# Kernel optimization log

Hardware: AMD Instinct MI355X
Metric: run time of the kernel (lower is better)

Reference implementation:

```python
import jax, jax.numpy as jnp
import numpy as np
import math

GROUPS = 32
EPS = 1e-5

def group_norm(x, w, b):
    B, C, H, W = x.shape
    xg = x.reshape(B, GROUPS, C // GROUPS, H, W)
    mu = xg.mean(axis=(2, 3, 4), keepdims=True)
    var = xg.var(axis=(2, 3, 4), keepdims=True)
    xn = ((xg - mu) * jax.lax.rsqrt(var + EPS)).reshape(B, C, H, W)
    return xn * w[None, :, None, None] + b[None, :, None, None]

def conv1x1(x, w, b):
    # x: [B,Cin,H,W], w: [Cout,Cin], b: [Cout]
    return jnp.einsum('bchw,oc->bohw', x, w) + b[None, :, None, None]

def setup_inputs() -> dict:
    key = jax.random.key(0)
    ks = jax.random.split(key, 8)
    B, C, E, H, W = 8, 256, 512, 64, 64
    x = jax.random.normal(ks[0], (B, C, H, W), dtype=jnp.float32)
    condA = jax.random.normal(ks[1], (B, E, H, W), dtype=jnp.float32)
    gn_x_w = jnp.ones((C,), jnp.float32)
    gn_x_b = jnp.zeros((C,), jnp.float32)
    gn_c_w = jnp.ones((E,), jnp.float32)
    gn_c_b = jnp.zeros((E,), jnp.float32)
    q_w = jax.random.normal(ks[2], (C, C), jnp.float32) * 0.02
    q_b = jnp.zeros((C,), jnp.float32)
    k_w = jax.random.normal(ks[3], (C, E), jnp.float32) * 0.02
    k_b = jnp.zeros((C,), jnp.float32)
    v_w = jax.random.normal(ks[4], (C, E), jnp.float32) * 0.02
    v_b = jnp.zeros((C,), jnp.float32)
    return {"x": x, "condA": condA, "gn_x_w": gn_x_w, "gn_x_b": gn_x_b,
            "gn_c_w": gn_c_w, "gn_c_b": gn_c_b, "q_w": q_w, "q_b": q_b,
            "k_w": k_w, "k_b": k_b, "v_w": v_w, "v_b": v_b}

def reference(x, condA, gn_x_w, gn_x_b, gn_c_w, gn_c_b, q_w, q_b, k_w, k_b, v_w, v_b):
    B, C, H, W = x.shape
    scale = math.sqrt(C)
    h = group_norm(x, gn_x_w, gn_x_b)
    h1 = group_norm(condA, gn_c_w, gn_c_b)
    q = conv1x1(h, q_w, q_b)      # [B,C,H,W]
    k = conv1x1(h1, k_w, k_b)     # [B,C,Hc,Wc]
    v = conv1x1(h1, v_w, v_b)     # [B,C,Hc,Wc]
    qf = q.transpose(0, 2, 3, 1).reshape(B, H * W, C)        # [B,N,C]
    kf = k.reshape(B, C, -1)                                  # [B,C,M]
    vf = v.transpose(0, 2, 3, 1).reshape(B, -1, C)            # [B,M,C]
    attn = jax.nn.softmax(jnp.einsum('bnc,bcm->bnm', qf, kf) / scale, axis=-1)
    out = jnp.einsum('bnm,bmc->bnc', attn, vf)                # [B,N,C]
    return out.reshape(B, H, W, C).transpose(0, 3, 1, 2)
```

## Files before the change

kernel.cpp:

```cpp
#include <hip/hip_runtime.h>


typedef _Float16 half8 __attribute__((ext_vector_type(8)));
typedef _Float16 half4v __attribute__((ext_vector_type(4)));
typedef _Float16 half2v __attribute__((ext_vector_type(2)));
typedef float f32x4 __attribute__((ext_vector_type(4)));
typedef float f32x16 __attribute__((ext_vector_type(16)));
typedef unsigned u32x4v __attribute__((ext_vector_type(4)));

#define MFMA16(a, b, c) __builtin_amdgcn_mfma_f32_16x16x32_f16((a), (b), (c), 0, 0, 0)
#define MFMA32(a, b, c) __builtin_amdgcn_mfma_f32_32x32x16_f16((a), (b), (c), 0, 0, 0)

__global__ __launch_bounds__(256) void statswconv_kernel(
    const float* __restrict__ x, const float* __restrict__ condA,
    float* __restrict__ sx, float* __restrict__ sc,
    const float* __restrict__ wq, const float* __restrict__ wk,
    const float* __restrict__ wv, _Float16* __restrict__ wqt,
    _Float16* __restrict__ wkt, _Float16* __restrict__ wvt) {
  int bid = blockIdx.x;
  int t = threadIdx.x;
  if (bid >= 512) {
    int i = (bid - 512) * 256 + t;
    const float* src;
    _Float16* dst;
    int cin, ksbits, gi;
    if (i < 8192) { src = wq; dst = wqt; cin = 256; ksbits = 3; gi = i; }
    else if (i < 24576) { src = wk; dst = wkt; cin = 512; ksbits = 4; gi = i - 8192; }
    else { src = wv; dst = wvt; cin = 512; ksbits = 4; gi = i - 24576; }
    int tile = gi >> 6, g = gi & 63;
    int otile = tile >> ksbits, ks = tile & ((1 << ksbits) - 1);
    int o = otile * 16 + (g & 15), k = ks * 32 + (g >> 4) * 8;
    const float* s = src + (size_t)o * cin + k;
    half8 hv;
#pragma unroll
    for (int j = 0; j < 8; j++) hv[j] = (_Float16)s[j];
    *(half8*)(dst + (size_t)gi * 8) = hv;
    return;
  }
  const float4* src;
  int nf4;
  float* dst;
  float inv_n;
  if (bid < 256) {
    src = (const float4*)(x + (size_t)bid * 32768);
    nf4 = 8192;
    dst = sx + bid * 2;
    inv_n = 1.0f / 32768.0f;
  } else {
    int j = bid - 256;
    src = (const float4*)(condA + (size_t)j * 65536);
    nf4 = 16384;
    dst = sc + j * 2;
    inv_n = 1.0f / 65536.0f;
  }
  float s = 0.f, s2 = 0.f;
  for (int i = t; i < nf4; i += 256) {
    float4 v = src[i];
    s += v.x + v.y + v.z + v.w;
    s2 += v.x * v.x + v.y * v.y + v.z * v.z + v.w * v.w;
  }
#pragma unroll
  for (int m = 1; m <= 32; m <<= 1) {
    s += __shfl_xor(s, m, 64);
    s2 += __shfl_xor(s2, m, 64);
  }
  __shared__ float red[8];
  int w = t >> 6;
  if ((t & 63) == 0) { red[w * 2] = s; red[w * 2 + 1] = s2; }
  __syncthreads();
  if (t == 0) {
    float S = red[0] + red[2] + red[4] + red[6];
    float S2 = red[1] + red[3] + red[5] + red[7];
    float mu = S * inv_n;
    float var = S2 * inv_n - mu * mu;
    dst[0] = mu;
    dst[1] = rsqrtf(var + 1e-5f);
  }
}

__global__ __launch_bounds__(256) void ntrans_kernel(
    const float* __restrict__ x, const float* __restrict__ condA,
    const float* __restrict__ statsx, const float* __restrict__ statsc,
    const float* __restrict__ gxw, const float* __restrict__ gxb,
    const float* __restrict__ gcw, const float* __restrict__ gcb,
    _Float16* __restrict__ hxTt, _Float16* __restrict__ h1Tt) {
  int bid = blockIdx.x;
  const float *src, *stats, *gw, *gb;
  _Float16* dst;
  int CH, gsh, bid2;
  if (bid < 2048) {
    src = x; stats = statsx; gw = gxw; gb = gxb; dst = hxTt;
    CH = 256; gsh = 3; bid2 = bid;
  } else {
    src = condA; stats = statsc; gw = gcw; gb = gcb; dst = h1Tt;
    CH = 512; gsh = 4; bid2 = bid - 2048;
  }
  int b = bid2 & 7, nt = (bid2 >> 3) & 63, ctile = bid2 >> 9;
  int n0 = nt * 64, c0 = ctile * 64;
  int t = threadIdx.x;
  __shared__ float tile[64][65];

  int cl = t >> 2;
  int c = c0 + cl;
  const float* st = stats + ((size_t)b * 32 + (c >> gsh)) * 2;
  float mu = st[0], rs = st[1];
  float a = rs * gw[c];
  float bb = gb[c] - mu * a;
  const float* srow = src + ((size_t)(b * CH + c)) * 4096 + n0 + (t & 3) * 16;
#pragma unroll
  for (int i = 0; i < 4; i++) {
    float4 v = *(const float4*)(srow + 4 * i);
    int nn = (t & 3) * 16 + 4 * i;
    tile[cl][nn + 0] = v.x * a + bb;
    tile[cl][nn + 1] = v.y * a + bb;
    tile[cl][nn + 2] = v.z * a + bb;
    tile[cl][nn + 3] = v.w * a + bb;
  }
  __syncthreads();
  int nl = t >> 2;
  half8 ov[2];
#pragma unroll
  for (int u = 0; u < 2; u++)
#pragma unroll
    for (int i = 0; i < 8; i++) ov[u][i] = (_Float16)tile[(t & 3) * 16 + 8 * u + i][nl];
  int n = n0 + nl;
  size_t tb = ((size_t)b * 256 + (n >> 4)) * (CH >> 5);
  int ca = c0 + (t & 3) * 16;
#pragma unroll
  for (int u = 0; u < 2; u++) {
    int cc = ca + 8 * u;
    size_t addr = ((tb + (cc >> 5)) * 64 + (n & 15) + 16 * ((cc >> 3) & 3)) * 8;
    *(half8*)(dst + addr) = ov[u];
  }
}

__global__ __launch_bounds__(256, 2) void projQ_kernel(
    const _Float16* __restrict__ Ht, const _Float16* __restrict__ Wt,
    const float* __restrict__ bias, _Float16* __restrict__ Qt) {
  int bid = blockIdx.x;
  int b = bid & 7, nt = bid >> 3;
  int t = threadIdx.x, l = t & 63, w = t >> 6;
  int c15 = l & 15, q = l >> 4;

  __shared__ __align__(16) _Float16 hbuf[16384];
  half8* hb = (half8*)hbuf;
  {
    const half8* sg = (const half8*)Ht + (size_t)(b * 256 + nt * 4) * 512;
#pragma unroll
    for (int i = 0; i < 8; i++) hb[t + 256 * i] = sg[t + 256 * i];
  }
  __syncthreads();

  const half8* wt8 = (const half8*)Wt;
#pragma unroll
  for (int p = 0; p < 2; p++) {
    int oa = (p * 4 + w) * 2;
    f32x4 acc[2][4] = {};
#pragma unroll
    for (int ks = 0; ks < 8; ks++) {
      half8 af0 = wt8[((size_t)(oa + 0) * 8 + ks) * 64 + l];
      half8 af1 = wt8[((size_t)(oa + 1) * 8 + ks) * 64 + l];
#pragma unroll
      for (int nt2 = 0; nt2 < 4; nt2++) {
        half8 bf = hb[(nt2 * 8 + ks) * 64 + l];
        acc[0][nt2] = MFMA16(af0, bf, acc[0][nt2]);
        acc[1][nt2] = MFMA16(af1, bf, acc[1][nt2]);
      }
    }
#pragma unroll
    for (int j = 0; j < 2; j++) {
      int o4 = (oa + j) * 16 + 4 * q;
      f32x4 bv = *(const f32x4*)(bias + o4);
#pragma unroll
      for (int nt2 = 0; nt2 < 4; nt2++) {
        half4v hv;
#pragma unroll
        for (int r = 0; r < 4; r++) hv[r] = (_Float16)((acc[j][nt2][r] + bv[r]) * 0.0625f);
        size_t addr = ((((size_t)b * 128 + nt * 2 + (nt2 >> 1)) * 16 + (oa + j)) * 64 +
                       (nt2 & 1) * 16 + c15 + 32 * (q >> 1)) * 8 + (q & 1) * 4;
        *(half4v*)(Qt + addr) = hv;
      }
    }
  }
}

__global__ __launch_bounds__(256, 2) void projKV_kernel(
    const _Float16* __restrict__ Ht, const _Float16* __restrict__ Wk,
    const _Float16* __restrict__ Wv, const float* __restrict__ kb,
    const float* __restrict__ vb, _Float16* __restrict__ Kt,
    _Float16* __restrict__ Vt) {
  int bid = blockIdx.x;
  int b = bid & 7, mt = bid >> 3;
  int m0 = mt * 64;
  int t = threadIdx.x, l = t & 63, w = t >> 6;
  int c15 = l & 15, q = l >> 4;

  __shared__ __align__(16) _Float16 hbuf[32768];
  half8* hb = (half8*)hbuf;
  {
    const half8* sg = (const half8*)Ht + (size_t)(b * 256 + mt * 4) * 1024;
#pragma unroll
    for (int i = 0; i < 16; i++) hb[t + 256 * i] = sg[t + 256 * i];
  }
  __syncthreads();

  const half8* wk8 = (const half8*)Wk;
  const half8* wv8 = (const half8*)Wv;
#pragma unroll
  for (int p = 0; p < 2; p++) {
    int oa = (p * 4 + w) * 2;
    f32x4 acck[2][4] = {};
    f32x4 accv[4][2] = {};
#pragma unroll
    for (int ks = 0; ks < 16; ks++) {
      half8 kf0 = wk8[((size_t)(oa + 0) * 16 + ks) * 64 + l];
      half8 kf1 = wk8[((size_t)(oa + 1) * 16 + ks) * 64 + l];
      half8 vf0 = wv8[((size_t)(oa + 0) * 16 + ks) * 64 + l];
      half8 vf1 = wv8[((size_t)(oa + 1) * 16 + ks) * 64 + l];
#pragma unroll
      for (int nt2 = 0; nt2 < 4; nt2++) {
        half8 lf = hb[(nt2 * 16 + ks) * 64 + l];
        acck[0][nt2] = MFMA16(kf0, lf, acck[0][nt2]);
        acck[1][nt2] = MFMA16(kf1, lf, acck[1][nt2]);
        accv[nt2][0] = MFMA16(lf, vf0, accv[nt2][0]);
        accv[nt2][1] = MFMA16(lf, vf1, accv[nt2][1]);
      }
    }
#pragma unroll
    for (int j = 0; j < 2; j++) {
      int o4 = (oa + j) * 16 + 4 * q;
      f32x4 bv = *(const f32x4*)(kb + o4);
#pragma unroll
      for (int nt2 = 0; nt2 < 4; nt2++) {
        half4v hv;
#pragma unroll
        for (int r = 0; r < 4; r++) hv[r] = (_Float16)(acck[j][nt2][r] + bv[r]);
        size_t addr = ((((size_t)b * 128 + mt * 2 + (nt2 >> 1)) * 16 + (oa + j)) * 64 +
                       (nt2 & 1) * 16 + c15 + 32 * (q >> 1)) * 8 + (q & 1) * 4;
        *(half4v*)(Kt + addr) = hv;
      }
    }
#pragma unroll
    for (int nt2 = 0; nt2 < 4; nt2++) {
      int m = m0 + nt2 * 16 + 4 * q;
      size_t mbase = ((size_t)b * 256 + (m >> 4)) * 8;
#pragma unroll
      for (int j = 0; j < 2; j++) {
        int c = (oa + j) * 16 + c15;
        float bs = vb[c];
        half4v hv;
#pragma unroll
        for (int r = 0; r < 4; r++) hv[r] = (_Float16)(accv[nt2][j][r] + bs);
        size_t addr = ((mbase + (c >> 5)) * 64 + (c & 31) + ((q >> 1) << 5)) * 8 + (q & 1) * 4;
        *(half4v*)(Vt + addr) = hv;
      }
    }
  }
}

__global__ __launch_bounds__(256, 2) void attn_kernel(
    const _Float16* __restrict__ Qt, const _Float16* __restrict__ Kt,
    const _Float16* __restrict__ Vt, float* __restrict__ out,
    float* __restrict__ O1, float* __restrict__ l0g,
    float* __restrict__ l1g) {
  int bid = blockIdx.x;
  int b = bid & 7, nt = bid >> 3;
  int n0 = nt * 64;
  int t = threadIdx.x, l = t & 63, w = t >> 6;
  int l31 = l & 31, h = l >> 5;
  int mh = w & 1, nh = w >> 1;

  __shared__ __align__(16) _Float16 qlds[16384];
  half8* ql8 = (half8*)qlds;
  {
    const half8* sg = (const half8*)Qt + (size_t)(b * 128 + nt * 2) * 1024;
#pragma unroll
    for (int i = 0; i < 8; i++) ql8[t + 256 * i] = sg[t + 256 * i];
  }
  __syncthreads();

  const half8* kt8 = (const half8*)Kt + (size_t)b * 131072 + mh * 1024 + l;
  const half8* vt8 = (const half8*)Vt + (size_t)b * 131072 + l;
  const half8* qw8 = ql8 + nh * 1024 + l;

  f32x16 acc[8] = {};
  float l_part = 0.f;

  for (int it = 0; it < 64; it++) {
    const half8* kb = kt8 + (size_t)it * 2048;

    f32x16 s = {};
#pragma unroll
    for (int g = 0; g < 4; g++) {
      half8 kf[4], qb[4];
#pragma unroll
      for (int i = 0; i < 4; i++) kf[i] = kb[(g * 4 + i) * 64];
#pragma unroll
      for (int i = 0; i < 4; i++) qb[i] = qw8[(g * 4 + i) * 64];
      __builtin_amdgcn_s_setprio(1);
#pragma unroll
      for (int i = 0; i < 4; i++) s = MFMA32(kf[i], qb[i], s);
      __builtin_amdgcn_s_setprio(0);
    }

    unsigned uo[8];
#pragma unroll
    for (int k2 = 0; k2 < 8; k2++) {
      float e0 = __expf(s[2 * k2]);
      float e1 = __expf(s[2 * k2 + 1]);
      l_part += e0 + e1;
      half2v h2 = {(_Float16)e0, (_Float16)e1};
      uo[k2] = __builtin_bit_cast(unsigned, h2);
    }
    unsigned x0 = uo[0], y0 = uo[2];
    asm("v_permlane32_swap_b32 %0, %1" : "+v"(x0), "+v"(y0));
    unsigned x1 = uo[1], y1 = uo[3];
    asm("v_permlane32_swap_b32 %0, %1" : "+v"(x1), "+v"(y1));
    unsigned x2 = uo[4], y2 = uo[6];
    asm("v_permlane32_swap_b32 %0, %1" : "+v"(x2), "+v"(y2));
    unsigned x3 = uo[5], y3 = uo[7];
    asm("v_permlane32_swap_b32 %0, %1" : "+v"(x3), "+v"(y3));
    u32x4v P0 = {x0, x1, y0, y1};
    u32x4v P1 = {x2, x3, y2, y3};
    half8 pf0 = __builtin_bit_cast(half8, P0);
    half8 pf1 = __builtin_bit_cast(half8, P1);

    const half8* vb0 = vt8 + (size_t)((it * 4 + mh * 2) * 8) * 64;
#pragma unroll
    for (int u = 0; u < 2; u++) {
      const half8* vb = vb0 + u * 512;
      half8 pfu = u ? pf1 : pf0;
#pragma unroll
      for (int g = 0; g < 2; g++) {
        half8 vf[4];
#pragma unroll
        for (int i = 0; i < 4; i++) vf[i] = vb[(g * 4 + i) * 64];
        __builtin_amdgcn_s_setprio(1);
#pragma unroll
        for (int i = 0; i < 4; i++)
          acc[g * 4 + i] = MFMA32(pfu, vf[i], acc[g * 4 + i]);
        __builtin_amdgcn_s_setprio(0);
      }
    }
  }

  {
    float v = l_part + __shfl_xor(l_part, 32, 64);
    float* lG = mh ? l1g : l0g;
    if (l < 32) lG[b * 4096 + n0 + nh * 32 + l] = v;
  }
  float* ob = mh ? O1 : out;
#pragma unroll
  for (int cb = 0; cb < 8; cb++) {
    int c = cb * 32 + l31;
    float* orow = ob + ((size_t)(b * 256 + c)) * 4096 + n0 + nh * 32 + 4 * h;
#pragma unroll
    for (int k2 = 0; k2 < 4; k2++) {
      f32x4 o4;
#pragma unroll
      for (int r = 0; r < 4; r++) o4[r] = acc[cb][4 * k2 + r];
      *(f32x4*)(orow + 8 * k2) = o4;
    }
  }
}

__global__ __launch_bounds__(256) void combine_kernel(
    float* __restrict__ out, const float* __restrict__ O1,
    const float* __restrict__ l0g, const float* __restrict__ l1g) {
  size_t i = (size_t)blockIdx.x * 256 + threadIdx.x;
  f32x4 a = ((const f32x4*)out)[i];
  f32x4 b4 = ((const f32x4*)O1)[i];
  int bidx = (int)(i >> 18);
  int n4 = (int)(i & 1023);
  f32x4 La = ((const f32x4*)l0g)[bidx * 1024 + n4];
  f32x4 Lb = ((const f32x4*)l1g)[bidx * 1024 + n4];
  f32x4 r;
#pragma unroll
  for (int j = 0; j < 4; j++) r[j] = (a[j] + b4[j]) / (La[j] + Lb[j]);
  ((f32x4*)out)[i] = r;
}

extern "C" void kernel_launch(void* const* d_in, const int* in_sizes, int n_in,
                              void* d_out, int out_size, void* d_ws,
                              size_t ws_size, hipStream_t stream) {
  const float* x = (const float*)d_in[0];
  const float* condA = (const float*)d_in[1];
  const float* gxw = (const float*)d_in[2];
  const float* gxb = (const float*)d_in[3];
  const float* gcw = (const float*)d_in[4];
  const float* gcb = (const float*)d_in[5];
  const float* qw = (const float*)d_in[6];
  const float* qb = (const float*)d_in[7];
  const float* kw = (const float*)d_in[8];
  const float* kb = (const float*)d_in[9];
  const float* vw = (const float*)d_in[10];
  const float* vb = (const float*)d_in[11];
  float* out = (float*)d_out;

  char* ws = (char*)d_ws;
  float* statsx = (float*)(ws);
  float* statsc = (float*)(ws + 2048);
  _Float16* wqt = (_Float16*)(ws + 4096);
  _Float16* wkt = (_Float16*)(ws + 135168);
  _Float16* wvt = (_Float16*)(ws + 397312);
  char* p = ws + 659456;
  _Float16* hxTt = (_Float16*)p; p += (size_t)8 * 4096 * 256 * 2;
  _Float16* h1Tt = (_Float16*)p; p += (size_t)8 * 4096 * 512 * 2;
  _Float16* Qt = (_Float16*)p;   p += (size_t)8 * 4096 * 256 * 2;
  _Float16* Kt = (_Float16*)p;   p += (size_t)8 * 4096 * 256 * 2;
  _Float16* Vt = (_Float16*)p;

  float* O1 = (float*)(ws + 659456);
  float* l0g = (float*)(ws + 659456 + (size_t)33554432);
  float* l1g = (float*)(ws + 659456 + (size_t)33554432 + 131072);

  statswconv_kernel<<<672, 256, 0, stream>>>(x, condA, statsx, statsc,
                                             qw, kw, vw, wqt, wkt, wvt);
  ntrans_kernel<<<6144, 256, 0, stream>>>(x, condA, statsx, statsc,
                                          gxw, gxb, gcw, gcb, hxTt, h1Tt);
  projQ_kernel<<<512, 256, 0, stream>>>(hxTt, wqt, qb, Qt);
  projKV_kernel<<<512, 256, 0, stream>>>(h1Tt, wkt, wvt, kb, vb, Kt, Vt);
  attn_kernel<<<512, 256, 0, stream>>>(Qt, Kt, Vt, out, O1, l0g, l1g);
  combine_kernel<<<8192, 256, 0, stream>>>(out, O1, l0g, l1g);
}
```

Baseline: 411.0 us.

## Double-buffer K/V tiles in LDS via async global-to-LDS loads in attention

The attention kernel now uses 512-thread blocks that each cover 128 query rows. Q fragments are held in registers instead of LDS. Each K and V tile is staged once per block into double-buffered LDS with global_load_lds, so the next tile's copy overlaps compute on the current one. This shares K/V global traffic across more query rows and hides load latency, at the cost of 128KB of LDS, higher register pressure from the Q fragments, a barrier per iteration, and half as many blocks.

```diff
diff --git a/kernel.cpp b/kernel.cpp
--- a/kernel.cpp
+++ b/kernel.cpp
@@ -10,6 +10,11 @@
 
 #define MFMA16(a, b, c) __builtin_amdgcn_mfma_f32_16x16x32_f16((a), (b), (c), 0, 0, 0)
 #define MFMA32(a, b, c) __builtin_amdgcn_mfma_f32_32x32x16_f16((a), (b), (c), 0, 0, 0)
+
+#define GLOAD_LDS(src, dst)                                                   \
+  __builtin_amdgcn_global_load_lds(                                           \
+      (const __attribute__((address_space(1))) unsigned*)(src),               \
+      (__attribute__((address_space(3))) unsigned*)(dst), 16, 0, 0)
 
 __global__ __launch_bounds__(256) void statswconv_kernel(
     const float* __restrict__ x, const float* __restrict__ condA,
@@ -258,48 +263,67 @@
   }
 }
 
-__global__ __launch_bounds__(256, 2) void attn_kernel(
+__global__ __launch_bounds__(512, 2) void attn_kernel(
     const _Float16* __restrict__ Qt, const _Float16* __restrict__ Kt,
     const _Float16* __restrict__ Vt, float* __restrict__ out,
     float* __restrict__ O1, float* __restrict__ l0g,
     float* __restrict__ l1g) {
   int bid = blockIdx.x;
-  int b = bid & 7, nt = bid >> 3;
-  int n0 = nt * 64;
+  int b = bid & 7, nt2 = bid >> 3;
+  int n0 = nt2 * 128;
   int t = threadIdx.x, l = t & 63, w = t >> 6;
   int l31 = l & 31, h = l >> 5;
   int mh = w & 1, nh = w >> 1;
 
-  __shared__ __align__(16) _Float16 qlds[16384];
-  half8* ql8 = (half8*)qlds;
+  __shared__ __align__(16) _Float16 kbuf[2][16384];
+  __shared__ __align__(16) _Float16 vbuf[2][16384];
+
+  half8 qf[16];
   {
-    const half8* sg = (const half8*)Qt + (size_t)(b * 128 + nt * 2) * 1024;
-#pragma unroll
-    for (int i = 0; i < 8; i++) ql8[t + 256 * i] = sg[t + 256 * i];
-  }
-  __syncthreads();
-
-  const half8* kt8 = (const half8*)Kt + (size_t)b * 131072 + mh * 1024 + l;
-  const half8* vt8 = (const half8*)Vt + (size_t)b * 131072 + l;
-  const half8* qw8 = ql8 + nh * 1024 + l;
+    const half8* qt8 =
+        (const half8*)Qt + ((size_t)(b * 128 + nt2 * 4 + nh) * 16) * 64 + l;
+#pragma unroll
+    for (int ks = 0; ks < 16; ks++) qf[ks] = qt8[ks * 64];
+  }
+
+  const _Float16* ksrc = Kt + (size_t)b * 1048576;
+  const _Float16* vsrc = Vt + (size_t)b * 1048576;
 
   f32x16 acc[8] = {};
   float l_part = 0.f;
 
+#define STAGE(it)                                                          \
+  {                                                                        \
+    int bs_ = (it) & 1;                                                    \
+    const _Float16* ks_ = ksrc + (size_t)(it) * 16384;                     \
+    const _Float16* vs_ = vsrc + (size_t)(it) * 16384;                     \
+    _Float16* kd_ = &kbuf[bs_][0];                                         \
+    _Float16* vd_ = &vbuf[bs_][0];                                         \
+    _Pragma("unroll") for (int r_ = 0; r_ < 4; r_++) {                     \
+      GLOAD_LDS(ks_ + (t + 512 * r_) * 8, kd_ + (t + 512 * r_) * 8);       \
+      GLOAD_LDS(vs_ + (t + 512 * r_) * 8, vd_ + (t + 512 * r_) * 8);       \
+    }                                                                      \
+  }
+
+  STAGE(0);
+  __syncthreads();
+
   for (int it = 0; it < 64; it++) {
-    const half8* kb = kt8 + (size_t)it * 2048;
+    int cur = it & 1;
+    if (it < 63) STAGE(it + 1);
+
+    const half8* kb = (const half8*)&kbuf[cur][0] + mh * 1024 + l;
+    const half8* vb8 = (const half8*)&vbuf[cur][0] + l;
 
     f32x16 s = {};
 #pragma unroll
     for (int g = 0; g < 4; g++) {
-      half8 kf[4], qb[4];
+      half8 kf[4];
 #pragma unroll
       for (int i = 0; i < 4; i++) kf[i] = kb[(g * 4 + i) * 64];
-#pragma unroll
-      for (int i = 0; i < 4; i++) qb[i] = qw8[(g * 4 + i) * 64];
       __builtin_amdgcn_s_setprio(1);
 #pragma unroll
-      for (int i = 0; i < 4; i++) s = MFMA32(kf[i], qb[i], s);
+      for (int i = 0; i < 4; i++) s = MFMA32(kf[i], qf[g * 4 + i], s);
       __builtin_amdgcn_s_setprio(0);
     }
 
@@ -325,16 +349,15 @@
     half8 pf0 = __builtin_bit_cast(half8, P0);
     half8 pf1 = __builtin_bit_cast(half8, P1);
 
-    const half8* vb0 = vt8 + (size_t)((it * 4 + mh * 2) * 8) * 64;
 #pragma unroll
     for (int u = 0; u < 2; u++) {
-      const half8* vb = vb0 + u * 512;
+      const half8* vv = vb8 + ((mh * 2 + u) * 8) * 64;
       half8 pfu = u ? pf1 : pf0;
 #pragma unroll
       for (int g = 0; g < 2; g++) {
         half8 vf[4];
 #pragma unroll
-        for (int i = 0; i < 4; i++) vf[i] = vb[(g * 4 + i) * 64];
+        for (int i = 0; i < 4; i++) vf[i] = vv[(g * 4 + i) * 64];
         __builtin_amdgcn_s_setprio(1);
 #pragma unroll
         for (int i = 0; i < 4; i++)
@@ -342,7 +365,9 @@
         __builtin_amdgcn_s_setprio(0);
       }
     }
-  }
+    __syncthreads();
+  }
+#undef STAGE
 
   {
     float v = l_part + __shfl_xor(l_part, 32, 64);
@@ -420,6 +445,6 @@
                                           gxw, gxb, gcw, gcb, hxTt, h1Tt);
   projQ_kernel<<<512, 256, 0, stream>>>(hxTt, wqt, qb, Qt);
   projKV_kernel<<<512, 256, 0, stream>>>(h1Tt, wkt, wvt, kb, vb, Kt, Vt);
-  attn_kernel<<<512, 256, 0, stream>>>(Qt, Kt, Vt, out, O1, l0g, l1g);
+  attn_kernel<<<256, 512, 0, stream>>>(Qt, Kt, Vt, out, O1, l0g, l1g);
   combine_kernel<<<8192, 256, 0, stream>>>(out, O1, l0g, l1g);
 }
```

Result: faster. 395.3 us (-3.8%).
